# Optimization experiments

Measured on AMD Instinct MI355X. Metric: run time of the kernel, lower is better.

Reference implementation:

```python
import jax, jax.numpy as jnp
import numpy as np

# model dims
N = 512        # node_size (ROIs)
S = 64         # sampling_size
TRS = 20       # TRs_per_window
STEPS = 20     # steps_per_TR = tr / step_size
DT = 0.05      # step_size (s)

# fixed Wong-Wang / Balloon-Windkessel constants (var=0 params in ParamsModel)
W_E, W_I = 1.0, 0.7
TAU_E, TAU_I = 0.1, 0.01
GAMMA_E, GAMMA_I = 0.641, 1.0
I_0, I_EXT = 0.32, 0.02
A_E, B_E, D_E = 310.0, 125.0, 0.16
A_I, B_I, D_I = 615.0, 177.0, 0.087
ALPHA, RHO = 0.32, 0.34
K1, K2, K3 = 2.38, 2.0, 0.48
V0, E0 = 0.02, 0.34
TAU_S, TAU_F, TAU_0 = 0.65, 0.41, 0.98


def h_tf(a, b, d, z):
    # abs-regularized sigmoid transfer (a*z-b)/(1-exp(-d*(a*z-b)))
    x = a * z - b
    return (1e-5 + jnp.abs(x)) / (1e-5 * d + jnp.abs(1.0 - jnp.exp(-d * x)))


def setup_inputs() -> dict:
    key = jax.random.key(0)
    ks = jax.random.split(key, 8)
    sc = jax.random.uniform(ks[0], (N, N), dtype=jnp.float32) * (1.0 - jnp.eye(N, dtype=jnp.float32))
    gains_con = 0.05 * jax.random.normal(ks[1], (N, N), dtype=jnp.float32)
    # hx: [N, 6] initial states (E, I, x, f, v, q)
    hx = jnp.concatenate([
        0.1 * jnp.ones((N, 2), jnp.float32),   # E, I
        jnp.zeros((N, 1), jnp.float32),        # x
        jnp.ones((N, 3), jnp.float32),         # f, v, q
    ], axis=1)
    hE = 0.1 * jnp.ones((N, 20), jnp.float32)
    external = jnp.zeros((N, STEPS, TRS), jnp.float32)
    noise_E0 = jax.random.normal(ks[2], (TRS, STEPS, N, S), dtype=jnp.float32)
    noise_I0 = jax.random.normal(ks[3], (TRS, STEPS, N, S), dtype=jnp.float32)
    noise_E = jax.random.normal(ks[4], (TRS, STEPS, N, S), dtype=jnp.float32)
    noise_I = jax.random.normal(ks[5], (TRS, STEPS, N, S), dtype=jnp.float32)
    noise_bold = jax.random.normal(ks[6], (TRS, N), dtype=jnp.float32)
    return dict(external=external, hx=hx, hE=hE, sc=sc, gains_con=gains_con,
                g=jnp.float32(20.0), g_EE=jnp.float32(3.5), g_IE=jnp.float32(0.42),
                g_EI=jnp.float32(0.42), std_in=jnp.float32(0.0), std_out=jnp.float32(0.02),
                noise_E0=noise_E0, noise_I0=noise_I0, noise_E=noise_E, noise_I=noise_I,
                noise_bold=noise_bold)


def reference(external, hx, hE, sc, gains_con, g, g_EE, g_IE, g_EI, std_in, std_out,
              noise_E0, noise_I0, noise_E, noise_I, noise_bold):
    relu = jax.nn.relu
    g_EE_e = 0.001 + relu(g_EE)
    g_IE_e = 0.001 + relu(g_IE)
    g_EI_e = 0.001 + relu(g_EI)
    std_in_e = 0.02 + relu(std_in)
    std_out_e = relu(std_out)
    # fitted, symmetrized, normalized SC -> Laplacian coupling
    sc_mod = jnp.exp(gains_con) * sc
    w = 0.5 * (sc_mod + sc_mod.T)
    w_n = w / jnp.linalg.norm(w)
    lap = -jnp.diag(w_n.sum(1)) + w_n                      # [N, N]
    ext = jnp.transpose(external, (2, 1, 0))               # [TRS, STEPS, N]
    sqdt = jnp.sqrt(jnp.float32(DT))

    def micro(carry, xs):
        hxE, hxI, x, f, v, q = carry
        e0, i0, eE, eI, ex = xs
        E = hxE[:, None] + 0.02 * e0                       # [N, S]
        I = hxI[:, None] + 0.001 * i0
        IE = jnp.tanh(relu(W_E * I_0 + I_EXT * ex[:, None] + g_EE_e * E + g * (lap @ E) - g_IE_e * I))
        II = jnp.tanh(relu(W_I * I_0 + g_EI_e * E - I))
        rE = h_tf(A_E, B_E, D_E, IE)
        rI = h_tf(A_I, B_I, D_I, II)
        En = E + DT * (-E / TAU_E + GAMMA_E * (1.0 - E) * rE) + sqdt * std_in_e * eE
        In = I + DT * (-I / TAU_I + GAMMA_I * rI) + sqdt * std_in_e * eI
        E = jnp.tanh(relu(En))                             # dynamic boundary
        I = jnp.tanh(relu(In))
        Em = jnp.maximum(E.mean(1), 1e-5)                  # [N]
        Im = jnp.maximum(I.mean(1), 1e-5)
        # hemodynamic (balloon-windkessel) states
        v_a = v ** (1.0 / ALPHA)
        xn = x + DT * (Em - x / TAU_S - (f - 1.0) / TAU_F)
        fn = f + DT * x
        vn = v + DT * (f - v_a) / TAU_0
        qn = q + DT * (f * (1.0 - (1.0 - RHO) ** (1.0 / f)) / RHO - q * v_a / v) / TAU_0
        return (Em, Im, jnp.tanh(xn), 1.0 + jnp.tanh(fn - 1.0),
                1.0 + jnp.tanh(vn - 1.0), 1.0 + jnp.tanh(qn - 1.0)), None

    def tr_step(carry, xs):
        e0, i0, eE, eI, exs, eb = xs
        carry, _ = jax.lax.scan(micro, carry, (e0, i0, eE, eI, exs))
        Em, Im, x, f, v, q = carry
        bold = std_out_e * eb + 100.0 * V0 / E0 * (K1 * (1.0 - q) + K2 * (1.0 - q / v) + K3 * (1.0 - v))
        return carry, bold

    carry0 = (hx[:, 0], hx[:, 1], hx[:, 2], hx[:, 3], hx[:, 4], hx[:, 5])
    _, bolds = jax.lax.scan(tr_step, carry0, (noise_E0, noise_I0, noise_E, noise_I, ext, noise_bold))
    return bolds.T                                         # [N, TRS] simulated BOLD window
```

## Files before the change

kernel.cpp:

```cpp
#include <hip/hip_runtime.h>
#include <hip/hip_bf16.h>

#define NN 512
#define SSAMP 64
#define NSTEP 400

__device__ __forceinline__ float wsum(float v){
  v += __shfl_xor(v, 32, 64);
  v += __shfl_xor(v, 16, 64);
  v += __shfl_xor(v,  8, 64);
  v += __shfl_xor(v,  4, 64);
  v += __shfl_xor(v,  2, 64);
  v += __shfl_xor(v,  1, 64);
  return v;
}
__device__ __forceinline__ float tanh_pos(float u){
  float e = __expf(2.0f*u);
  return 1.0f - 2.0f/(e+1.0f);
}
__device__ __forceinline__ float tanh_gen(float u){
  float a = fabsf(u);
  float e = __expf(2.0f*a);
  float t = 1.0f - 2.0f/(e+1.0f);
  return copysignf(t, u);
}
__device__ __forceinline__ float h_tf(float a, float b, float d, float z){
  float x = fmaf(a, z, -b);
  float num = 1e-5f + fabsf(x);
  float den = 1e-5f*d + fabsf(1.0f - __expf(-d*x));
  return num/den;
}

__device__ __forceinline__ float l0_load(const float* p){ return *p; }
__device__ __forceinline__ float l0_load(const __hip_bfloat16* p){ return __bfloat162float(*p); }
__device__ __forceinline__ void  l0_store(float* p, float v){ *p = v; }
__device__ __forceinline__ void  l0_store(__hip_bfloat16* p, float v){ *p = __float2bfloat16(v); }

#define F4ELEM(v,m) ((m)==0?(v).x:(m)==1?(v).y:(m)==2?(v).z:(v).w)

__global__ __launch_bounds__(256) void prep_w_kernel(
    const float* __restrict__ sc, const float* __restrict__ gc,
    float* __restrict__ w, float* __restrict__ normsq){
  int idx = blockIdx.x*256 + threadIdx.x;
  int i = idx >> 9, j = idx & 511;
  float a = __expf(gc[idx])*sc[idx];
  float b = __expf(gc[j*NN+i])*sc[j*NN+i];
  float wij = 0.5f*(a + b);
  w[idx] = wij;
  float p = wsum(wij*wij);
  if ((threadIdx.x & 63) == 0) atomicAdd(normsq, p);
}

__global__ __launch_bounds__(64) void prep_lap_kernel(
    const float* __restrict__ w, const float* __restrict__ normsq,
    float* __restrict__ lap){
  int i = blockIdx.x;
  int l = threadIdx.x;
  float vals[8]; float s = 0.f;
  #pragma unroll
  for (int j=0;j<8;j++){ vals[j] = w[i*NN + j*64 + l]; s += vals[j]; }
  float rs = wsum(s);
  float rn = 1.0f/sqrtf(normsq[0]);
  #pragma unroll
  for (int j=0;j<8;j++){
    int col = j*64 + l;
    float x = vals[j] - (col==i ? rs : 0.0f);
    lap[i*NN+col] = x*rn;
  }
}

template<typename TL>
__global__ __launch_bounds__(256) void gemm_kernel(
    const float* __restrict__ lap, const float* __restrict__ nE0,
    TL* __restrict__ L0){
  __shared__ __align__(16) float e0s[64][64];
  int t = blockIdx.y;
  int tid = threadIdx.x;
  int ts = tid & 7, tr = tid >> 3;
  int r0 = blockIdx.x*128 + tr*4;
  int s0 = ts*8;
  const float* e0t = nE0 + (size_t)t*NN*SSAMP;
  float acc[4][8];
  #pragma unroll
  for (int i=0;i<4;i++)
    #pragma unroll
    for (int j=0;j<8;j++) acc[i][j]=0.f;

  for (int kt=0; kt<8; ++kt){
    int kr = tid>>4, c4 = (tid&15)*4;
    const float* src = e0t + (size_t)(kt*64+kr)*SSAMP + c4;
    float4 a0 = *(const float4*)(src);
    float4 a1 = *(const float4*)(src + 16*SSAMP);
    float4 a2 = *(const float4*)(src + 32*SSAMP);
    float4 a3 = *(const float4*)(src + 48*SSAMP);
    __syncthreads();
    *(float4*)(&e0s[kr   ][c4]) = a0;
    *(float4*)(&e0s[kr+16][c4]) = a1;
    *(float4*)(&e0s[kr+32][c4]) = a2;
    *(float4*)(&e0s[kr+48][c4]) = a3;
    __syncthreads();
    const float* lb = lap + (size_t)r0*NN + kt*64;
    for (int kk=0; kk<64; kk+=4){
      float4 lq0 = *(const float4*)(lb +        kk);
      float4 lq1 = *(const float4*)(lb +   NN + kk);
      float4 lq2 = *(const float4*)(lb + 2*NN + kk);
      float4 lq3 = *(const float4*)(lb + 3*NN + kk);
      #pragma unroll
      for (int m=0;m<4;m++){
        float lm[4] = {F4ELEM(lq0,m), F4ELEM(lq1,m), F4ELEM(lq2,m), F4ELEM(lq3,m)};
        float4 ea = *(const float4*)(&e0s[kk+m][s0]);
        float4 eb = *(const float4*)(&e0s[kk+m][s0+4]);
        float ev[8] = {ea.x,ea.y,ea.z,ea.w, eb.x,eb.y,eb.z,eb.w};
        #pragma unroll
        for (int i=0;i<4;i++)
          #pragma unroll
          for (int j=0;j<8;j++)
            acc[i][j] = fmaf(lm[i], ev[j], acc[i][j]);
      }
    }
  }
  #pragma unroll
  for (int i=0;i<4;i++){
    TL* dst = L0 + ((size_t)t*NN + r0 + i)*SSAMP + s0;
    #pragma unroll
    for (int j=0;j<8;j++) l0_store(&dst[j], acc[i][j]);
  }
}

template<typename TL>
__global__ __launch_bounds__(256) void seq_kernel(
    const float* __restrict__ external, const float* __restrict__ hx,
    const float* __restrict__ lap, const TL* __restrict__ L0,
    const float* __restrict__ nE0, const float* __restrict__ nI0,
    const float* __restrict__ nE,  const float* __restrict__ nI,
    const float* __restrict__ nB,
    const float* __restrict__ gp,   const float* __restrict__ gEEp,
    const float* __restrict__ gIEp, const float* __restrict__ gEIp,
    const float* __restrict__ stdinp, const float* __restrict__ stdoutp,
    unsigned long long* __restrict__ xbuf,
    float* __restrict__ out)
{
  __shared__ float hxs[NN];
  const int tid  = threadIdx.x;
  const int wv   = tid >> 6, lane = tid & 63;
  const int n    = blockIdx.x*4 + wv;

  const float g    = gp[0];
  const float gEE  = 0.001f + fmaxf(gEEp[0], 0.f);
  const float gIE  = 0.001f + fmaxf(gIEp[0], 0.f);
  const float gEI  = 0.001f + fmaxf(gEIp[0], 0.f);
  const float sdin = 0.02f  + fmaxf(stdinp[0], 0.f);
  const float sdout=          fmaxf(stdoutp[0], 0.f);
  const float sqin = 0.22360679774997896f * sdin;

  float hxE = hx[n*6+0], hxI = hx[n*6+1];
  float xs  = hx[n*6+2], fs  = hx[n*6+3], vs = hx[n*6+4], qs = hx[n*6+5];

  if (lane==0){
    unsigned long long pk = (1ULL<<32) | (unsigned long long)__float_as_uint(hxE);
    __hip_atomic_store(&xbuf[n], pk, __ATOMIC_RELAXED, __HIP_MEMORY_SCOPE_AGENT);
  }

  const size_t nsbase = (size_t)n*SSAMP + lane;
  float c_e0 = nE0[nsbase];
  float c_i0 = nI0[nsbase];
  float c_eE = nE [nsbase];
  float c_eI = nI [nsbase];
  float c_L0 = l0_load(&L0[nsbase]);
  float c_ex = external[n*400 + 0];

  const float* laprow = lap + (size_t)n*NN;

  #pragma unroll 1
  for (int t=0; t<NSTEP; ++t){
    int tn = (t+1 < NSTEP) ? t+1 : t;
    size_t offn = (size_t)tn*NN*SSAMP + nsbase;
    float p_e0 = nE0[offn], p_i0 = nI0[offn], p_eE = nE[offn], p_eI = nI[offn];
    float p_L0 = l0_load(&L0[offn]);
    float p_ex = external[n*400 + (tn%20)*20 + (tn/20)];

    float E = fmaf(0.02f , c_e0, hxE);
    float I = fmaf(0.001f, c_i0, hxI);
    float II = tanh_pos(fmaxf(fmaf(gEI, E, 0.224f) - I, 0.f));
    float rI = h_tf(615.0f, 177.0f, 0.087f, II);
    float In = I + 0.05f*fmaf(-100.0f, I, rI) + sqin*c_eI;
    float Ip = tanh_pos(fmaxf(In, 0.f));
    float Im = fmaxf(wsum(Ip)*0.015625f, 1e-5f);
    float IEpre = 0.32f + 0.02f*c_ex + gEE*E + g*0.02f*c_L0 - gIE*I;

    const unsigned long long want = (unsigned long long)(t+1);
    unsigned long long* bc = xbuf + (size_t)(t&1)*NN;
    unsigned long long u0, u1;
    for(;;){
      u0 = __hip_atomic_load(&bc[tid],     __ATOMIC_RELAXED, __HIP_MEMORY_SCOPE_AGENT);
      u1 = __hip_atomic_load(&bc[tid+256], __ATOMIC_RELAXED, __HIP_MEMORY_SCOPE_AGENT);
      int ok = (int)(((u0>>32)==want) & ((u1>>32)==want));
      if (__syncthreads_and(ok)) break;
    }
    hxs[tid]     = __uint_as_float((unsigned int)u0);
    hxs[tid+256] = __uint_as_float((unsigned int)u1);
    __syncthreads();

    float mv = 0.f;
    #pragma unroll
    for (int j=0;j<8;j++) mv = fmaf(laprow[j*64+lane], hxs[j*64+lane], mv);
    float lapHx = wsum(mv);

    float IE = tanh_pos(fmaxf(fmaf(g, lapHx, IEpre), 0.f));
    float rE = h_tf(310.0f, 125.0f, 0.16f, IE);
    float En = E + 0.05f*fmaf(0.641f*(1.0f-E), rE, -10.0f*E) + sqin*c_eE;
    float Ep = tanh_pos(fmaxf(En, 0.f));
    float Em = fmaxf(wsum(Ep)*0.015625f, 1e-5f);

    if (lane==0){
      unsigned long long pk = ((unsigned long long)(t+2)<<32)
                            | (unsigned long long)__float_as_uint(Em);
      __hip_atomic_store(&xbuf[(size_t)((t+1)&1)*NN + n], pk,
                         __ATOMIC_RELAXED, __HIP_MEMORY_SCOPE_AGENT);
    }

    float va = __expf(3.125f*__logf(vs));
    float xn = xs + 0.05f*(Em - xs*1.5384615384615385f - (fs-1.0f)*2.4390243902439024f);
    float fn = fs + 0.05f*xs;
    float vn = vs + 0.05f*(fs - va)*1.0204081632653061f;
    float qn = qs + 0.05f*( fs*(1.0f - __expf(-0.41551544396166582f/fs))*2.9411764705882355f
                            - qs*va/vs )*1.0204081632653061f;
    xs = tanh_gen(xn);
    fs = 1.0f + tanh_gen(fn - 1.0f);
    vs = 1.0f + tanh_gen(vn - 1.0f);
    qs = 1.0f + tanh_gen(qn - 1.0f);
    hxE = Em; hxI = Im;

    if (((t+1) % 20) == 0 && lane==0){
      int tr = t/20;
      float eb = nB[tr*NN + n];
      float bold = sdout*eb + 5.882352941176471f*( 2.38f*(1.0f-qs)
                   + 2.0f*(1.0f - qs/vs) + 0.48f*(1.0f-vs) );
      out[n*20 + tr] = bold;
    }

    c_e0=p_e0; c_i0=p_i0; c_eE=p_eE; c_eI=p_eI; c_L0=p_L0; c_ex=p_ex;
  }
}

extern "C" void kernel_launch(void* const* d_in, const int* in_sizes, int n_in,
                              void* d_out, int out_size, void* d_ws, size_t ws_size,
                              hipStream_t stream) {
  (void)in_sizes; (void)n_in; (void)out_size;
  const float* external = (const float*)d_in[0];
  const float* hx   = (const float*)d_in[1];
  const float* sc   = (const float*)d_in[3];
  const float* gc   = (const float*)d_in[4];
  const float* gp   = (const float*)d_in[5];
  const float* gEE  = (const float*)d_in[6];
  const float* gIE  = (const float*)d_in[7];
  const float* gEI  = (const float*)d_in[8];
  const float* stdi = (const float*)d_in[9];
  const float* stdo = (const float*)d_in[10];
  const float* nE0  = (const float*)d_in[11];
  const float* nI0  = (const float*)d_in[12];
  const float* nE   = (const float*)d_in[13];
  const float* nI   = (const float*)d_in[14];
  const float* nB   = (const float*)d_in[15];
  float* out = (float*)d_out;

  char* ws = (char*)d_ws;
  float* normsq = (float*)ws;
  unsigned long long* xbuf = (unsigned long long*)(ws + 256);
  float* w   = (float*)(ws + 16384);
  float* lap = (float*)(ws + 16384 + (1<<20));
  char*  l0p = ws + 16384 + (2<<20);

  hipMemsetAsync(ws, 0, 16384, stream);
  prep_w_kernel  <<<1024, 256, 0, stream>>>(sc, gc, w, normsq);
  prep_lap_kernel<<< 512,  64, 0, stream>>>(w, normsq, lap);

  size_t l0_f32  = (size_t)NSTEP*NN*SSAMP*sizeof(float);
  size_t need_f32 = 16384 + (2<<20) + l0_f32;
  if (ws_size >= need_f32){
    gemm_kernel<float><<<dim3(4,NSTEP), 256, 0, stream>>>(lap, nE0, (float*)l0p);
    seq_kernel<float><<<128, 256, 0, stream>>>(external, hx, lap, (const float*)l0p,
        nE0, nI0, nE, nI, nB, gp, gEE, gIE, gEI, stdi, stdo, xbuf, out);
  } else {
    gemm_kernel<__hip_bfloat16><<<dim3(4,NSTEP), 256, 0, stream>>>(lap, nE0, (__hip_bfloat16*)l0p);
    seq_kernel<__hip_bfloat16><<<128, 256, 0, stream>>>(external, hx, lap, (const __hip_bfloat16*)l0p,
        nE0, nI0, nE, nI, nB, gp, gEE, gIE, gEI, stdi, stdo, xbuf, out);
  }
}
```

Before: 1.157 ms.

## Use split-bf16 MFMA GEMM for L0 and per-wave 32-bit packed barrier

Replaces the FP32 SIMT GEMM that precomputes lap·noise_E0 with a matrix-core path. Both operands are split into bf16 hi/lo pairs (three MFMA products to keep near-fp32 accuracy), and noise_E0 is pre-transposed. The sequential kernel's cross-block exchange now packs an 8-bit step tag with a 24-bit truncated float into 32-bit words. Each wave polls all 512 entries itself with __all instead of a block-wide syncthreads_and plus shared-memory staging, and Laplacian rows are held in registers. This adds extra prep kernels and workspace, and truncates the exchanged E values to 24 bits.

```diff
diff --git a/kernel.cpp b/kernel.cpp
--- a/kernel.cpp
+++ b/kernel.cpp
@@ -4,6 +4,9 @@
 #define NN 512
 #define SSAMP 64
 #define NSTEP 400
+
+typedef __attribute__((ext_vector_type(4))) float f32x4;
+typedef __attribute__((ext_vector_type(8))) short s16x8;
 
 __device__ __forceinline__ float wsum(float v){
   v += __shfl_xor(v, 32, 64);
@@ -30,11 +33,13 @@
   float den = 1e-5f*d + fabsf(1.0f - __expf(-d*x));
   return num/den;
 }
-
-__device__ __forceinline__ float l0_load(const float* p){ return *p; }
-__device__ __forceinline__ float l0_load(const __hip_bfloat16* p){ return __bfloat162float(*p); }
-__device__ __forceinline__ void  l0_store(float* p, float v){ *p = v; }
-__device__ __forceinline__ void  l0_store(__hip_bfloat16* p, float v){ *p = __float2bfloat16(v); }
+__device__ __forceinline__ unsigned pack24(float v, unsigned tag){
+  unsigned fb = __float_as_uint(v);
+  return (tag<<24) | ((fb + 0x80u) >> 8);
+}
+__device__ __forceinline__ float unpack24(unsigned u){
+  return __uint_as_float(u << 8);
+}
 
 #define F4ELEM(v,m) ((m)==0?(v).x:(m)==1?(v).y:(m)==2?(v).z:(v).w)
 
@@ -69,10 +74,94 @@
   }
 }
 
-template<typename TL>
-__global__ __launch_bounds__(256) void gemm_kernel(
+__global__ __launch_bounds__(256) void lap_split_kernel(
+    const float* __restrict__ lap,
+    __hip_bfloat16* __restrict__ lh, __hip_bfloat16* __restrict__ ll){
+  int i = blockIdx.x*256 + threadIdx.x;
+  float f = lap[i];
+  __hip_bfloat16 h = __float2bfloat16(f);
+  lh[i] = h;
+  ll[i] = __float2bfloat16(f - __bfloat162float(h));
+}
+
+__global__ __launch_bounds__(256) void e0t_kernel(
+    const float* __restrict__ nE0,
+    __hip_bfloat16* __restrict__ th, __hip_bfloat16* __restrict__ tl){
+  __shared__ float tile[64][65];
+  int t = blockIdx.y, c = blockIdx.x;
+  const float* src = nE0 + ((size_t)t*NN + c*64)*SSAMP;
+  int tid = threadIdx.x;
+  int r0 = tid>>2, c4 = (tid&3)*16;
+  #pragma unroll
+  for (int i=0;i<4;i++){
+    float4 v = *(const float4*)(src + r0*64 + c4 + i*4);
+    tile[r0][c4+i*4+0]=v.x; tile[r0][c4+i*4+1]=v.y;
+    tile[r0][c4+i*4+2]=v.z; tile[r0][c4+i*4+3]=v.w;
+  }
+  __syncthreads();
+  int s = tid>>2, nseg = (tid&3)*16;
+  __hip_bfloat16 hs[16], ls[16];
+  #pragma unroll
+  for (int i=0;i<16;i++){
+    float f = tile[nseg+i][s];
+    __hip_bfloat16 h = __float2bfloat16(f);
+    hs[i] = h;
+    ls[i] = __float2bfloat16(f - __bfloat162float(h));
+  }
+  size_t doff = ((size_t)t*64 + s)*NN + c*64 + nseg;
+  *(uint4*)(th + doff)     = *(uint4*)&hs[0];
+  *(uint4*)(th + doff + 8) = *(uint4*)&hs[8];
+  *(uint4*)(tl + doff)     = *(uint4*)&ls[0];
+  *(uint4*)(tl + doff + 8) = *(uint4*)&ls[8];
+}
+
+__global__ __launch_bounds__(256) void mfma_gemm_kernel(
+    const __hip_bfloat16* __restrict__ Ah, const __hip_bfloat16* __restrict__ Al,
+    const __hip_bfloat16* __restrict__ Bh, const __hip_bfloat16* __restrict__ Bl,
+    float* __restrict__ L0){
+  int t = blockIdx.y;
+  int nb = blockIdx.x;
+  int w  = threadIdx.x>>6, l = threadIdx.x&63;
+  int lr = l&15, lg = l>>4;
+  f32x4 acc[4][2] = {};
+  const short* ahp = (const short*)Ah + ((size_t)t*64 + lr)*NN + lg*8;
+  const short* alp = (const short*)Al + ((size_t)t*64 + lr)*NN + lg*8;
+  int col0 = nb*128 + w*32 + lr;
+  const short* bhp = (const short*)Bh + (size_t)col0*NN + lg*8;
+  const short* blp = (const short*)Bl + (size_t)col0*NN + lg*8;
+  for (int k0=0; k0<NN; k0+=32){
+    s16x8 a_h[4], a_l[4], b_h[2], b_l[2];
+    #pragma unroll
+    for (int mt=0;mt<4;mt++){
+      a_h[mt] = *(const s16x8*)(ahp + mt*16*NN + k0);
+      a_l[mt] = *(const s16x8*)(alp + mt*16*NN + k0);
+    }
+    #pragma unroll
+    for (int nt=0;nt<2;nt++){
+      b_h[nt] = *(const s16x8*)(bhp + nt*16*NN + k0);
+      b_l[nt] = *(const s16x8*)(blp + nt*16*NN + k0);
+    }
+    #pragma unroll
+    for (int mt=0;mt<4;mt++)
+      #pragma unroll
+      for (int nt=0;nt<2;nt++){
+        acc[mt][nt] = __builtin_amdgcn_mfma_f32_16x16x32_bf16(a_h[mt], b_h[nt], acc[mt][nt],0,0,0);
+        acc[mt][nt] = __builtin_amdgcn_mfma_f32_16x16x32_bf16(a_l[mt], b_h[nt], acc[mt][nt],0,0,0);
+        acc[mt][nt] = __builtin_amdgcn_mfma_f32_16x16x32_bf16(a_h[mt], b_l[nt], acc[mt][nt],0,0,0);
+      }
+  }
+  #pragma unroll
+  for (int mt=0;mt<4;mt++)
+    #pragma unroll
+    for (int nt=0;nt<2;nt++){
+      float* dst = L0 + ((size_t)t*NN + nb*128 + w*32 + nt*16 + lr)*SSAMP + mt*16 + lg*4;
+      *(f32x4*)dst = acc[mt][nt];
+    }
+}
+
+__global__ __launch_bounds__(256) void gemm_fallback_kernel(
     const float* __restrict__ lap, const float* __restrict__ nE0,
-    TL* __restrict__ L0){
+    float* __restrict__ L0){
   __shared__ __align__(16) float e0s[64][64];
   int t = blockIdx.y;
   int tid = threadIdx.x;
@@ -85,7 +174,6 @@
   for (int i=0;i<4;i++)
     #pragma unroll
     for (int j=0;j<8;j++) acc[i][j]=0.f;
-
   for (int kt=0; kt<8; ++kt){
     int kr = tid>>4, c4 = (tid&15)*4;
     const float* src = e0t + (size_t)(kt*64+kr)*SSAMP + c4;
@@ -121,26 +209,24 @@
   }
   #pragma unroll
   for (int i=0;i<4;i++){
-    TL* dst = L0 + ((size_t)t*NN + r0 + i)*SSAMP + s0;
-    #pragma unroll
-    for (int j=0;j<8;j++) l0_store(&dst[j], acc[i][j]);
-  }
-}
-
-template<typename TL>
+    float* dst = L0 + ((size_t)t*NN + r0 + i)*SSAMP + s0;
+    #pragma unroll
+    for (int j=0;j<8;j++) dst[j] = acc[i][j];
+  }
+}
+
 __global__ __launch_bounds__(256) void seq_kernel(
     const float* __restrict__ external, const float* __restrict__ hx,
-    const float* __restrict__ lap, const TL* __restrict__ L0,
+    const float* __restrict__ lap, const float* __restrict__ L0,
     const float* __restrict__ nE0, const float* __restrict__ nI0,
     const float* __restrict__ nE,  const float* __restrict__ nI,
     const float* __restrict__ nB,
     const float* __restrict__ gp,   const float* __restrict__ gEEp,
     const float* __restrict__ gIEp, const float* __restrict__ gEIp,
     const float* __restrict__ stdinp, const float* __restrict__ stdoutp,
-    unsigned long long* __restrict__ xbuf,
+    unsigned* __restrict__ xbuf,
     float* __restrict__ out)
 {
-  __shared__ float hxs[NN];
   const int tid  = threadIdx.x;
   const int wv   = tid >> 6, lane = tid & 63;
   const int n    = blockIdx.x*4 + wv;
@@ -156,27 +242,28 @@
   float hxE = hx[n*6+0], hxI = hx[n*6+1];
   float xs  = hx[n*6+2], fs  = hx[n*6+3], vs = hx[n*6+4], qs = hx[n*6+5];
 
-  if (lane==0){
-    unsigned long long pk = (1ULL<<32) | (unsigned long long)__float_as_uint(hxE);
-    __hip_atomic_store(&xbuf[n], pk, __ATOMIC_RELAXED, __HIP_MEMORY_SCOPE_AGENT);
-  }
+  float lr[8];
+  #pragma unroll
+  for (int j=0;j<8;j++) lr[j] = lap[(size_t)n*NN + j*64 + lane];
+
+  if (lane==0)
+    __hip_atomic_store(&xbuf[n], pack24(hxE, 1u),
+                       __ATOMIC_RELAXED, __HIP_MEMORY_SCOPE_AGENT);
 
   const size_t nsbase = (size_t)n*SSAMP + lane;
   float c_e0 = nE0[nsbase];
   float c_i0 = nI0[nsbase];
   float c_eE = nE [nsbase];
   float c_eI = nI [nsbase];
-  float c_L0 = l0_load(&L0[nsbase]);
+  float c_L0 = L0 [nsbase];
   float c_ex = external[n*400 + 0];
-
-  const float* laprow = lap + (size_t)n*NN;
 
   #pragma unroll 1
   for (int t=0; t<NSTEP; ++t){
     int tn = (t+1 < NSTEP) ? t+1 : t;
     size_t offn = (size_t)tn*NN*SSAMP + nsbase;
     float p_e0 = nE0[offn], p_i0 = nI0[offn], p_eE = nE[offn], p_eI = nI[offn];
-    float p_L0 = l0_load(&L0[offn]);
+    float p_L0 = L0[offn];
     float p_ex = external[n*400 + (tn%20)*20 + (tn/20)];
 
     float E = fmaf(0.02f , c_e0, hxE);
@@ -188,22 +275,22 @@
     float Im = fmaxf(wsum(Ip)*0.015625f, 1e-5f);
     float IEpre = 0.32f + 0.02f*c_ex + gEE*E + g*0.02f*c_L0 - gIE*I;
 
-    const unsigned long long want = (unsigned long long)(t+1);
-    unsigned long long* bc = xbuf + (size_t)(t&1)*NN;
-    unsigned long long u0, u1;
+    const unsigned want = (unsigned)(t+1) & 0xFFu;
+    unsigned* bc = xbuf + (size_t)(t&1)*NN;
+    unsigned u[8];
     for(;;){
-      u0 = __hip_atomic_load(&bc[tid],     __ATOMIC_RELAXED, __HIP_MEMORY_SCOPE_AGENT);
-      u1 = __hip_atomic_load(&bc[tid+256], __ATOMIC_RELAXED, __HIP_MEMORY_SCOPE_AGENT);
-      int ok = (int)(((u0>>32)==want) & ((u1>>32)==want));
-      if (__syncthreads_and(ok)) break;
-    }
-    hxs[tid]     = __uint_as_float((unsigned int)u0);
-    hxs[tid+256] = __uint_as_float((unsigned int)u1);
-    __syncthreads();
+      #pragma unroll
+      for (int j=0;j<8;j++)
+        u[j] = __hip_atomic_load(&bc[j*64+lane], __ATOMIC_RELAXED, __HIP_MEMORY_SCOPE_AGENT);
+      int ok = 1;
+      #pragma unroll
+      for (int j=0;j<8;j++) ok &= (int)((u[j]>>24) == want);
+      if (__all(ok)) break;
+    }
 
     float mv = 0.f;
     #pragma unroll
-    for (int j=0;j<8;j++) mv = fmaf(laprow[j*64+lane], hxs[j*64+lane], mv);
+    for (int j=0;j<8;j++) mv = fmaf(lr[j], unpack24(u[j]), mv);
     float lapHx = wsum(mv);
 
     float IE = tanh_pos(fmaxf(fmaf(g, lapHx, IEpre), 0.f));
@@ -212,12 +299,10 @@
     float Ep = tanh_pos(fmaxf(En, 0.f));
     float Em = fmaxf(wsum(Ep)*0.015625f, 1e-5f);
 
-    if (lane==0){
-      unsigned long long pk = ((unsigned long long)(t+2)<<32)
-                            | (unsigned long long)__float_as_uint(Em);
-      __hip_atomic_store(&xbuf[(size_t)((t+1)&1)*NN + n], pk,
+    if (lane==0)
+      __hip_atomic_store(&xbuf[(size_t)((t+1)&1)*NN + n],
+                         pack24(Em, (unsigned)(t+2) & 0xFFu),
                          __ATOMIC_RELAXED, __HIP_MEMORY_SCOPE_AGENT);
-    }
 
     float va = __expf(3.125f*__logf(vs));
     float xn = xs + 0.05f*(Em - xs*1.5384615384615385f - (fs-1.0f)*2.4390243902439024f);
@@ -265,25 +350,30 @@
   float* out = (float*)d_out;
 
   char* ws = (char*)d_ws;
-  float* normsq = (float*)ws;
-  unsigned long long* xbuf = (unsigned long long*)(ws + 256);
-  float* w   = (float*)(ws + 16384);
-  float* lap = (float*)(ws + 16384 + (1<<20));
-  char*  l0p = ws + 16384 + (2<<20);
-
-  hipMemsetAsync(ws, 0, 16384, stream);
+  const size_t MB = 1048576;
+  float*    normsq = (float*)ws;
+  unsigned* xbuf   = (unsigned*)(ws + 256);
+  float* w    = (float*)(ws + 8192);
+  float* lap  = (float*)(ws + 8192 + 1*MB);
+  __hip_bfloat16* lh = (__hip_bfloat16*)(ws + 8192 + 2*MB);
+  __hip_bfloat16* ll = (__hip_bfloat16*)(ws + 8192 + 2*MB + 512*1024);
+  float* L0 = (float*)(ws + 8192 + 3*MB);
+  size_t l0b = (size_t)NSTEP*NN*SSAMP*sizeof(float);
+  __hip_bfloat16* th = (__hip_bfloat16*)(ws + 8192 + 3*MB + l0b);
+  __hip_bfloat16* tl = th + (size_t)NSTEP*64*NN;
+
+  hipMemsetAsync(ws, 0, 8192, stream);
   prep_w_kernel  <<<1024, 256, 0, stream>>>(sc, gc, w, normsq);
   prep_lap_kernel<<< 512,  64, 0, stream>>>(w, normsq, lap);
 
-  size_t l0_f32  = (size_t)NSTEP*NN*SSAMP*sizeof(float);
-  size_t need_f32 = 16384 + (2<<20) + l0_f32;
-  if (ws_size >= need_f32){
-    gemm_kernel<float><<<dim3(4,NSTEP), 256, 0, stream>>>(lap, nE0, (float*)l0p);
-    seq_kernel<float><<<128, 256, 0, stream>>>(external, hx, lap, (const float*)l0p,
-        nE0, nI0, nE, nI, nB, gp, gEE, gIE, gEI, stdi, stdo, xbuf, out);
+  size_t need_full = 8192 + 3*MB + l0b + 2*(size_t)NSTEP*64*NN*sizeof(__hip_bfloat16);
+  if (ws_size >= need_full){
+    lap_split_kernel<<<1024, 256, 0, stream>>>(lap, lh, ll);
+    e0t_kernel<<<dim3(8, NSTEP), 256, 0, stream>>>(nE0, th, tl);
+    mfma_gemm_kernel<<<dim3(4, NSTEP), 256, 0, stream>>>(th, tl, lh, ll, L0);
   } else {
-    gemm_kernel<__hip_bfloat16><<<dim3(4,NSTEP), 256, 0, stream>>>(lap, nE0, (__hip_bfloat16*)l0p);
-    seq_kernel<__hip_bfloat16><<<128, 256, 0, stream>>>(external, hx, lap, (const __hip_bfloat16*)l0p,
-        nE0, nI0, nE, nI, nB, gp, gEE, gIE, gEI, stdi, stdo, xbuf, out);
-  }
-}
+    gemm_fallback_kernel<<<dim3(4, NSTEP), 256, 0, stream>>>(lap, nE0, L0);
+  }
+  seq_kernel<<<128, 256, 0, stream>>>(external, hx, lap, L0,
+      nE0, nI0, nE, nI, nB, gp, gEE, gIE, gEI, stdi, stdo, xbuf, out);
+}
```

Result: no change. 1.152 ms (-0.4%).
